# Kernel optimization log

Measured on AMD Instinct MI355X. Metric: run time of the kernel, lower is better.

The kernel has to match this reference:

```python
import jax, jax.numpy as jnp
import numpy as np

N_HEADS = 16
D_EMBED = 1024
D_HEAD = D_EMBED // N_HEADS
CAUSAL = False


def setup_inputs() -> dict:
    key = jax.random.key(0)
    k1, k2, k3, k4, k5 = jax.random.split(key, 5)
    B, S, D = 4, 2048, D_EMBED
    scale = 1.0 / np.sqrt(D)
    return {
        "x": jax.random.normal(k1, (B, S, D), dtype=jnp.float32),
        "w_in": jax.random.normal(k2, (D, 3 * D), dtype=jnp.float32) * scale,
        "b_in": jax.random.normal(k3, (3 * D,), dtype=jnp.float32) * 0.02,
        "w_out": jax.random.normal(k4, (D, D), dtype=jnp.float32) * scale,
        "b_out": jax.random.normal(k5, (D,), dtype=jnp.float32) * 0.02,
    }


def reference(x, w_in, b_in, w_out, b_out):
    B, S, D = x.shape
    qkv = jnp.einsum("bsd,de->bse", x, w_in) + b_in  # [B,S,3D]
    q, k, v = jnp.split(qkv, 3, axis=-1)
    # split heads -> [B,H,S,Dh]
    def sh(t):
        return t.reshape(B, S, N_HEADS, D_HEAD).transpose(0, 2, 1, 3)
    q, k, v = sh(q), sh(k), sh(v)
    weight = jnp.einsum("bhsd,bhtd->bhst", q, k)  # [B,H,S,S]
    if CAUSAL:
        mask = jnp.triu(jnp.ones((S, S), dtype=bool), k=1)
        weight = jnp.where(mask, -jnp.inf, weight)
    weight = weight / np.sqrt(D_HEAD)
    weight = jax.nn.softmax(weight, axis=-1)
    out = jnp.einsum("bhst,bhtd->bhsd", weight, v)
    out = out.transpose(0, 2, 1, 3).reshape(B, S, D)
    return jnp.einsum("bsd,de->bse", out, w_out) + b_out
```

## Files before the change

kernel.cpp:

```cpp
#include <hip/hip_runtime.h>
#include <hip/hip_bf16.h>

typedef unsigned short u16;
typedef __attribute__((ext_vector_type(8))) short bf16x8;
typedef __attribute__((ext_vector_type(4))) float f32x4;

#define QSCALE 0.180336880f

#define DEV static __device__ __forceinline__

DEV u16 f2bf(float f) {
  union { float f; unsigned u; } v; v.f = f;
  unsigned r = v.u + 0x7fffu + ((v.u >> 16) & 1u);
  return (u16)(r >> 16);
}

DEV unsigned pk2(float a, float b) {
  union { __hip_bfloat162 h; unsigned u; } c;
  c.h = __float22bfloat162_rn(make_float2(a, b));
  return c.u;
}

DEV void gll16(void* lds, const void* g) {
  __builtin_amdgcn_global_load_lds(
      (const __attribute__((address_space(1))) unsigned int*)g,
      (__attribute__((address_space(3))) unsigned int*)lds, 16, 0, 0);
}

DEV bf16x8 lds_swz_read(const u16* tile, int row, int colbyte) {
  const char* p = (const char*)tile + row * 128 + (colbyte ^ ((row & 7) << 4));
  return *(const bf16x8*)p;
}

DEV void stage_swz(u16* lds_tile, const u16* gbase, int gstride, int wave, int lane) {
#pragma unroll
  for (int j = 0; j < 2; ++j) {
    const int chunk = wave * 2 + j;
    const int a = chunk * 1024 + lane * 16;
    const int r = a >> 7;
    const int cb = (a & 127) ^ ((r & 7) << 4);
    gll16(lds_tile + chunk * 512, &gbase[(size_t)r * gstride + (cb >> 1)]);
  }
}

__global__ __launch_bounds__(256) void cvt_f32_to_bf16(const float* __restrict__ in,
                                                       u16* __restrict__ out, int n4) {
  int i = blockIdx.x * blockDim.x + threadIdx.x;
  int stride = gridDim.x * blockDim.x;
  for (; i < n4; i += stride) {
    float4 f = ((const float4*)in)[i];
    ushort4 u;
    u.x = f2bf(f.x); u.y = f2bf(f.y); u.z = f2bf(f.z); u.w = f2bf(f.w);
    ((ushort4*)out)[i] = u;
  }
}

__global__ __launch_bounds__(256) void transpose_cvt(const float* __restrict__ W,
                                                     u16* __restrict__ Wt,
                                                     int K, int N, int sn, float sval) {
  __shared__ u16 t[64][65];
  const int k0 = blockIdx.x * 64, n0 = blockIdx.y * 64;
  const int tid = threadIdx.x;
  const int rr = tid >> 4;
  const int cc = (tid & 15) * 4;
  const float scl = (n0 < sn) ? sval : 1.0f;
#pragma unroll
  for (int i = 0; i < 4; ++i) {
    const int row = rr * 4 + i;
    float4 f = *(const float4*)&W[(size_t)(k0 + row) * N + n0 + cc];
    t[row][cc + 0] = f2bf(f.x * scl);
    t[row][cc + 1] = f2bf(f.y * scl);
    t[row][cc + 2] = f2bf(f.z * scl);
    t[row][cc + 3] = f2bf(f.w * scl);
  }
  __syncthreads();
#pragma unroll
  for (int i = 0; i < 4; ++i) {
    const int n = rr * 4 + i;
    ushort4 u;
    u.x = t[cc + 0][n]; u.y = t[cc + 1][n]; u.z = t[cc + 2][n]; u.w = t[cc + 3][n];
    *(ushort4*)&Wt[(size_t)(n0 + n) * K + k0 + cc] = u;
  }
}

__global__ __launch_bounds__(256) void transpose_v(const u16* __restrict__ qkv,
                                                   u16* __restrict__ vT) {
  __shared__ u16 t[64][72];
  const int bh = blockIdx.y;
  const int b = bh >> 4, h = bh & 15;
  const int t0 = blockIdx.x * 64;
  const int tid = threadIdx.x;
  const int row = tid >> 2;
  const int cg = (tid & 3) * 16;
  const size_t src = (size_t)b * 2048 * 3072 + (size_t)(t0 + row) * 3072 + 2048 + h * 64 + cg;
  bf16x8 v0 = *(const bf16x8*)&qkv[src];
  bf16x8 v1 = *(const bf16x8*)&qkv[src + 8];
#pragma unroll
  for (int i = 0; i < 8; ++i) { t[row][cg + i] = (u16)v0[i]; t[row][cg + 8 + i] = (u16)v1[i]; }
  __syncthreads();
  const int d = tid >> 2;
  const int tg = (tid & 3) * 16;
  bf16x8 o0, o1;
#pragma unroll
  for (int i = 0; i < 8; ++i) { o0[i] = (short)t[tg + i][d]; o1[i] = (short)t[tg + 8 + i][d]; }
  u16* dst = &vT[((size_t)bh * 64 + d) * 2048 + t0 + tg];
  *(bf16x8*)dst = o0;
  *(bf16x8*)(dst + 8) = o1;
}

template<bool OUT_BF16>
__global__ __launch_bounds__(256) void gemm_bf16(const u16* __restrict__ A,
                                                 const u16* __restrict__ Bt,
                                                 const float* __restrict__ bias,
                                                 void* __restrict__ Cout,
                                                 int M, int N, int K, int qn) {
  __shared__ __align__(16) u16 As[128][64];
  __shared__ __align__(16) u16 Bs[128][64];
  const int tid = threadIdx.x;
  const int wave = tid >> 6, lane = tid & 63;
  const int g = lane >> 4, lr = lane & 15;
  const int bm = blockIdx.x * 128, bn = blockIdx.y * 128;
  const int wm = (wave >> 1) * 64, wn = (wave & 1) * 64;
  f32x4 acc[4][4] = {};
  for (int kt = 0; kt < K; kt += 64) {
    __syncthreads();
#pragma unroll
    for (int j = 0; j < 4; ++j) {
      int chunk = wave * 4 + j;
      int e = chunk * 512 + lane * 8;
      int r = e >> 6, c = e & 63;
      gll16((u16*)As + chunk * 512, &A[(size_t)(bm + r) * K + kt + c]);
      gll16((u16*)Bs + chunk * 512, &Bt[(size_t)(bn + r) * K + kt + c]);
    }
    __syncthreads();
#pragma unroll
    for (int kk = 0; kk < 64; kk += 32) {
      bf16x8 af[4], bfr[4];
#pragma unroll
      for (int m = 0; m < 4; ++m)
        af[m] = *(const bf16x8*)&As[wm + m * 16 + lr][kk + g * 8];
#pragma unroll
      for (int n = 0; n < 4; ++n)
        bfr[n] = *(const bf16x8*)&Bs[wn + n * 16 + lr][kk + g * 8];
#pragma unroll
      for (int m = 0; m < 4; ++m)
#pragma unroll
        for (int n = 0; n < 4; ++n)
          acc[m][n] = __builtin_amdgcn_mfma_f32_16x16x32_bf16(af[m], bfr[n], acc[m][n], 0, 0, 0);
    }
  }
#pragma unroll
  for (int m = 0; m < 4; ++m) {
#pragma unroll
    for (int n = 0; n < 4; ++n) {
      const int col = bn + wn + n * 16 + lr;
      float bv = bias ? bias[col] : 0.f;
      if (col < qn) bv *= QSCALE;
#pragma unroll
      for (int r = 0; r < 4; ++r) {
        const int row = bm + wm + m * 16 + g * 4 + r;
        float v = acc[m][n][r] + bv;
        if (OUT_BF16) ((u16*)Cout)[(size_t)row * N + col] = f2bf(v);
        else          ((float*)Cout)[(size_t)row * N + col] = v;
      }
    }
  }
}

__global__ __launch_bounds__(256) void attn_kernel(const u16* __restrict__ qkv,
                                                   const u16* __restrict__ vT,
                                                   u16* __restrict__ out) {
  __shared__ __align__(16) u16 Ks[2][4096];
  __shared__ __align__(16) u16 Vs[2][4096];
  __shared__ __align__(16) u16 Ps[4][1024];
  const int tid = threadIdx.x;
  const int wave = tid >> 6, lane = tid & 63;
  const int g = lane >> 4, lr = lane & 15;
  const int bh = blockIdx.y;
  const int b = bh >> 4, h = bh & 15;
  const int q0 = blockIdx.x * 64;
  const size_t base = (size_t)b * 2048 * 3072;
  const u16* kg = qkv + base + 1024 + h * 64;
  const u16* vg = vT + (size_t)bh * 64 * 2048;

  const int qrow = q0 + wave * 16 + lr;
  bf16x8 qf[2];
#pragma unroll
  for (int kk = 0; kk < 2; ++kk)
    qf[kk] = *(const bf16x8*)&qkv[base + (size_t)qrow * 3072 + h * 64 + kk * 32 + g * 8];

  f32x4 o[4] = {};
  float m = -1e30f, lsum = 0.f;

  stage_swz(Ks[0], kg, 3072, wave, lane);
  stage_swz(Vs[0], vg, 2048, wave, lane);
  __syncthreads();
  int cur = 0;
  char* const pwrow = (char*)Ps[wave] + lr * 128;
  const int psw = (lr & 7) << 4;
  for (int it = 0; it < 32; ++it) {
    if (it < 31) {
      stage_swz(Ks[cur ^ 1], kg + (size_t)(it + 1) * 64 * 3072, 3072, wave, lane);
      stage_swz(Vs[cur ^ 1], vg + (it + 1) * 64, 2048, wave, lane);
    }
    f32x4 s[4] = {};
#pragma unroll
    for (int kk = 0; kk < 2; ++kk)
#pragma unroll
      for (int n = 0; n < 4; ++n) {
        bf16x8 kf = lds_swz_read(Ks[cur], n * 16 + lr, kk * 64 + g * 16);
        s[n] = __builtin_amdgcn_mfma_f32_16x16x32_bf16(kf, qf[kk], s[n], 0, 0, 0);
      }
    f32x4 t01, t23;
#pragma unroll
    for (int i = 0; i < 4; ++i) {
      t01[i] = fmaxf(s[0][i], s[1][i]);
      t23[i] = fmaxf(s[2][i], s[3][i]);
    }
    f32x4 t = { fmaxf(t01[0], t23[0]), fmaxf(t01[1], t23[1]),
                fmaxf(t01[2], t23[2]), fmaxf(t01[3], t23[3]) };
    float pmax = fmaxf(fmaxf(t[0], t[1]), fmaxf(t[2], t[3]));
    if (!__all(pmax <= m + 8.f)) {
      float pm = fmaxf(pmax, __shfl_xor(pmax, 16));
      pm = fmaxf(pm, __shfl_xor(pm, 32));
      float mnew = fmaxf(m, pm);
      float sc = __builtin_amdgcn_exp2f(m - mnew);
      float sc0 = __shfl(sc, g * 4 + 0);
      float sc1 = __shfl(sc, g * 4 + 1);
      float sc2 = __shfl(sc, g * 4 + 2);
      float sc3 = __shfl(sc, g * 4 + 3);
#pragma unroll
      for (int nd = 0; nd < 4; ++nd) {
        o[nd][0] *= sc0; o[nd][1] *= sc1; o[nd][2] *= sc2; o[nd][3] *= sc3;
      }
      lsum *= sc;
      m = mnew;
    }
    float su = 0.f;
#pragma unroll
    for (int n = 0; n < 4; ++n) {
      float p0 = __builtin_amdgcn_exp2f(s[n][0] - m);
      float p1 = __builtin_amdgcn_exp2f(s[n][1] - m);
      float p2 = __builtin_amdgcn_exp2f(s[n][2] - m);
      float p3 = __builtin_amdgcn_exp2f(s[n][3] - m);
      uint2 w;
      w.x = pk2(p0, p1);
      w.y = pk2(p2, p3);
      *(uint2*)(pwrow + ((n * 32 + g * 8) ^ psw)) = w;
      su += (p0 + p1) + (p2 + p3);
    }
    lsum += su;
#pragma unroll
    for (int kk = 0; kk < 2; ++kk) {
      bf16x8 pf = lds_swz_read(Ps[wave], lr, kk * 64 + g * 16);
#pragma unroll
      for (int nd = 0; nd < 4; ++nd) {
        bf16x8 vf = lds_swz_read(Vs[cur], nd * 16 + lr, kk * 64 + g * 16);
        o[nd] = __builtin_amdgcn_mfma_f32_16x16x32_bf16(pf, vf, o[nd], 0, 0, 0);
      }
    }
    __syncthreads();
    cur ^= 1;
  }
  float lf = lsum + __shfl_xor(lsum, 16);
  lf += __shfl_xor(lf, 32);
  float l0 = __shfl(lf, g * 4 + 0);
  float l1 = __shfl(lf, g * 4 + 1);
  float l2 = __shfl(lf, g * 4 + 2);
  float l3 = __shfl(lf, g * 4 + 3);
  const size_t orow0 = (size_t)b * 2048 + q0 + wave * 16;
#pragma unroll
  for (int nd = 0; nd < 4; ++nd) {
    const int dcol = h * 64 + nd * 16 + lr;
    out[(orow0 + g * 4 + 0) * 1024 + dcol] = f2bf(o[nd][0] / l0);
    out[(orow0 + g * 4 + 1) * 1024 + dcol] = f2bf(o[nd][1] / l1);
    out[(orow0 + g * 4 + 2) * 1024 + dcol] = f2bf(o[nd][2] / l2);
    out[(orow0 + g * 4 + 3) * 1024 + dcol] = f2bf(o[nd][3] / l3);
  }
}

extern "C" void kernel_launch(void* const* d_in, const int* in_sizes, int n_in,
                              void* d_out, int out_size, void* d_ws, size_t ws_size,
                              hipStream_t stream) {
  (void)in_sizes; (void)n_in; (void)out_size; (void)ws_size;
  const float* x     = (const float*)d_in[0];
  const float* w_in  = (const float*)d_in[1];
  const float* b_in  = (const float*)d_in[2];
  const float* w_out = (const float*)d_in[3];
  const float* b_out = (const float*)d_in[4];
  float* out = (float*)d_out;

  char* ws = (char*)d_ws;
  u16* Xbf   = (u16*)ws; ws += (size_t)8192 * 1024 * 2;
  u16* WinT  = (u16*)ws; ws += (size_t)3072 * 1024 * 2;
  u16* WoutT = (u16*)ws; ws += (size_t)1024 * 1024 * 2;
  u16* qkv   = (u16*)ws; ws += (size_t)8192 * 3072 * 2;
  u16* attno = (u16*)ws; ws += (size_t)8192 * 1024 * 2;
  u16* vT    = Xbf;

  cvt_f32_to_bf16<<<2048, 256, 0, stream>>>(x, Xbf, 8192 * 1024 / 4);
  transpose_cvt<<<dim3(16, 48), 256, 0, stream>>>(w_in, WinT, 1024, 3072, 1024, QSCALE);
  transpose_cvt<<<dim3(16, 16), 256, 0, stream>>>(w_out, WoutT, 1024, 1024, 0, 1.0f);
  gemm_bf16<true ><<<dim3(64, 24), 256, 0, stream>>>(Xbf,   WinT,  b_in,  qkv, 8192, 3072, 1024, 1024);
  transpose_v<<<dim3(32, 64), 256, 0, stream>>>(qkv, vT);
  attn_kernel<<<dim3(32, 64), 256, 0, stream>>>(qkv, vT, attno);
  gemm_bf16<false><<<dim3(64, 8),  256, 0, stream>>>(attno, WoutT, b_out, out, 8192, 1024, 1024, 0);
}
```

Baseline: 265.0 us.

## Fuse V transpose into QKV GEMM epilogue and unroll attention loop by two

```diff
diff --git a/kernel.cpp b/kernel.cpp
--- a/kernel.cpp
+++ b/kernel.cpp
@@ -25,22 +25,6 @@
   __builtin_amdgcn_global_load_lds(
       (const __attribute__((address_space(1))) unsigned int*)g,
       (__attribute__((address_space(3))) unsigned int*)lds, 16, 0, 0);
-}
-
-DEV bf16x8 lds_swz_read(const u16* tile, int row, int colbyte) {
-  const char* p = (const char*)tile + row * 128 + (colbyte ^ ((row & 7) << 4));
-  return *(const bf16x8*)p;
-}
-
-DEV void stage_swz(u16* lds_tile, const u16* gbase, int gstride, int wave, int lane) {
-#pragma unroll
-  for (int j = 0; j < 2; ++j) {
-    const int chunk = wave * 2 + j;
-    const int a = chunk * 1024 + lane * 16;
-    const int r = a >> 7;
-    const int cb = (a & 127) ^ ((r & 7) << 4);
-    gll16(lds_tile + chunk * 512, &gbase[(size_t)r * gstride + (cb >> 1)]);
-  }
 }
 
 __global__ __launch_bounds__(256) void cvt_f32_to_bf16(const float* __restrict__ in,
@@ -113,7 +97,8 @@
                                                  const u16* __restrict__ Bt,
                                                  const float* __restrict__ bias,
                                                  void* __restrict__ Cout,
-                                                 int M, int N, int K, int qn) {
+                                                 int M, int N, int K, int qn,
+                                                 u16* __restrict__ vTout, int vn0) {
   __shared__ __align__(16) u16 As[128][64];
   __shared__ __align__(16) u16 Bs[128][64];
   const int tid = threadIdx.x;
@@ -156,16 +141,96 @@
       const int col = bn + wn + n * 16 + lr;
       float bv = bias ? bias[col] : 0.f;
       if (col < qn) bv *= QSCALE;
-#pragma unroll
-      for (int r = 0; r < 4; ++r) {
-        const int row = bm + wm + m * 16 + g * 4 + r;
-        float v = acc[m][n][r] + bv;
-        if (OUT_BF16) ((u16*)Cout)[(size_t)row * N + col] = f2bf(v);
-        else          ((float*)Cout)[(size_t)row * N + col] = v;
+      if (vTout != nullptr && col >= vn0) {
+        const int hc = col - vn0;
+#pragma unroll
+        for (int r = 0; r < 4; ++r) {
+          const int row = bm + wm + m * 16 + g * 4 + r;
+          const size_t idx = (((size_t)(row >> 11) * 16 + (hc >> 6)) * 64 + (hc & 63)) * 2048
+                             + (row & 2047);
+          vTout[idx] = f2bf(acc[m][n][r] + bv);
+        }
+      } else {
+#pragma unroll
+        for (int r = 0; r < 4; ++r) {
+          const int row = bm + wm + m * 16 + g * 4 + r;
+          float v = acc[m][n][r] + bv;
+          if (OUT_BF16) ((u16*)Cout)[(size_t)row * N + col] = f2bf(v);
+          else          ((float*)Cout)[(size_t)row * N + col] = v;
+        }
       }
     }
   }
 }
+
+
+#define ATTN_BODY(BUF, PRE)                                                     \
+  {                                                                             \
+    if (PRE) {                                                                  \
+      gll16((u16*)Ks[(BUF) ^ 1] + c0 * 512, gk0); gk0 += 64 * 3072;             \
+      gll16((u16*)Ks[(BUF) ^ 1] + c1 * 512, gk1); gk1 += 64 * 3072;             \
+      gll16((u16*)Vs[(BUF) ^ 1] + c0 * 512, gv0); gv0 += 64;                    \
+      gll16((u16*)Vs[(BUF) ^ 1] + c1 * 512, gv1); gv1 += 64;                    \
+    }                                                                           \
+    const char* kb = (const char*)Ks[(BUF)];                                    \
+    const char* vb = (const char*)Vs[(BUF)];                                    \
+    f32x4 s[4] = {};                                                            \
+    _Pragma("unroll")                                                           \
+    for (int kk = 0; kk < 2; ++kk)                                              \
+      _Pragma("unroll")                                                         \
+      for (int n = 0; n < 4; ++n) {                                             \
+        bf16x8 kf = *(const bf16x8*)(kb + off[kk][n]);                          \
+        s[n] = __builtin_amdgcn_mfma_f32_16x16x32_bf16(kf, qf[kk], s[n], 0, 0, 0); \
+      }                                                                         \
+    f32x4 t01, t23;                                                             \
+    _Pragma("unroll")                                                           \
+    for (int i = 0; i < 4; ++i) {                                               \
+      t01[i] = fmaxf(s[0][i], s[1][i]);                                         \
+      t23[i] = fmaxf(s[2][i], s[3][i]);                                         \
+    }                                                                           \
+    float pmax = fmaxf(fmaxf(fmaxf(t01[0], t23[0]), fmaxf(t01[1], t23[1])),     \
+                       fmaxf(fmaxf(t01[2], t23[2]), fmaxf(t01[3], t23[3])));    \
+    if (!__all(pmax <= m + 8.f)) {                                              \
+      float pm = fmaxf(pmax, __shfl_xor(pmax, 16));                             \
+      pm = fmaxf(pm, __shfl_xor(pm, 32));                                       \
+      float mnew = fmaxf(m, pm);                                                \
+      float sc = __builtin_amdgcn_exp2f(m - mnew);                              \
+      float sc0 = __shfl(sc, g * 4 + 0);                                        \
+      float sc1 = __shfl(sc, g * 4 + 1);                                        \
+      float sc2 = __shfl(sc, g * 4 + 2);                                        \
+      float sc3 = __shfl(sc, g * 4 + 3);                                        \
+      _Pragma("unroll")                                                         \
+      for (int nd = 0; nd < 4; ++nd) {                                          \
+        o[nd][0] *= sc0; o[nd][1] *= sc1; o[nd][2] *= sc2; o[nd][3] *= sc3;     \
+      }                                                                         \
+      lsum *= sc;                                                               \
+      m = mnew;                                                                 \
+    }                                                                           \
+    float su = 0.f;                                                             \
+    _Pragma("unroll")                                                           \
+    for (int n = 0; n < 4; ++n) {                                               \
+      float p0 = __builtin_amdgcn_exp2f(s[n][0] - m);                           \
+      float p1 = __builtin_amdgcn_exp2f(s[n][1] - m);                           \
+      float p2 = __builtin_amdgcn_exp2f(s[n][2] - m);                           \
+      float p3 = __builtin_amdgcn_exp2f(s[n][3] - m);                           \
+      uint2 w;                                                                  \
+      w.x = pk2(p0, p1);                                                        \
+      w.y = pk2(p2, p3);                                                        \
+      *(uint2*)(pb + pwo[n]) = w;                                               \
+      su += (p0 + p1) + (p2 + p3);                                              \
+    }                                                                           \
+    lsum += su;                                                                 \
+    _Pragma("unroll")                                                           \
+    for (int kk = 0; kk < 2; ++kk) {                                            \
+      bf16x8 pf = *(const bf16x8*)(pb + off[kk][0]);                            \
+      _Pragma("unroll")                                                         \
+      for (int nd = 0; nd < 4; ++nd) {                                          \
+        bf16x8 vf = *(const bf16x8*)(vb + off[kk][nd]);                         \
+        o[nd] = __builtin_amdgcn_mfma_f32_16x16x32_bf16(pf, vf, o[nd], 0, 0, 0); \
+      }                                                                         \
+    }                                                                           \
+    __syncthreads();                                                            \
+  }
 
 __global__ __launch_bounds__(256) void attn_kernel(const u16* __restrict__ qkv,
                                                    const u16* __restrict__ vT,
@@ -189,79 +254,42 @@
   for (int kk = 0; kk < 2; ++kk)
     qf[kk] = *(const bf16x8*)&qkv[base + (size_t)qrow * 3072 + h * 64 + kk * 32 + g * 8];
 
+  const int sw = (lr & 7) << 4;
+  int off[2][4];
+#pragma unroll
+  for (int kk = 0; kk < 2; ++kk)
+#pragma unroll
+    for (int n = 0; n < 4; ++n)
+      off[kk][n] = (n * 16 + lr) * 128 + ((kk * 64 + g * 16) ^ sw);
+  int pwo[4];
+#pragma unroll
+  for (int n = 0; n < 4; ++n)
+    pwo[n] = lr * 128 + ((n * 32 + g * 8) ^ sw);
+  char* const pb = (char*)Ps[wave];
+
+  const int c0 = wave * 2, c1 = c0 + 1;
+  const int a0 = c0 * 1024 + lane * 16, a1 = c1 * 1024 + lane * 16;
+  const int r0 = a0 >> 7, r1 = a1 >> 7;
+  const int cb0 = (a0 & 127) ^ ((r0 & 7) << 4), cb1 = (a1 & 127) ^ ((r1 & 7) << 4);
+  const u16* gk0 = kg + (size_t)r0 * 3072 + (cb0 >> 1);
+  const u16* gk1 = kg + (size_t)r1 * 3072 + (cb1 >> 1);
+  const u16* gv0 = vg + (size_t)r0 * 2048 + (cb0 >> 1);
+  const u16* gv1 = vg + (size_t)r1 * 2048 + (cb1 >> 1);
+
   f32x4 o[4] = {};
   float m = -1e30f, lsum = 0.f;
 
-  stage_swz(Ks[0], kg, 3072, wave, lane);
-  stage_swz(Vs[0], vg, 2048, wave, lane);
+  gll16((u16*)Ks[0] + c0 * 512, gk0); gk0 += 64 * 3072;
+  gll16((u16*)Ks[0] + c1 * 512, gk1); gk1 += 64 * 3072;
+  gll16((u16*)Vs[0] + c0 * 512, gv0); gv0 += 64;
+  gll16((u16*)Vs[0] + c1 * 512, gv1); gv1 += 64;
   __syncthreads();
-  int cur = 0;
-  char* const pwrow = (char*)Ps[wave] + lr * 128;
-  const int psw = (lr & 7) << 4;
-  for (int it = 0; it < 32; ++it) {
-    if (it < 31) {
-      stage_swz(Ks[cur ^ 1], kg + (size_t)(it + 1) * 64 * 3072, 3072, wave, lane);
-      stage_swz(Vs[cur ^ 1], vg + (it + 1) * 64, 2048, wave, lane);
-    }
-    f32x4 s[4] = {};
-#pragma unroll
-    for (int kk = 0; kk < 2; ++kk)
-#pragma unroll
-      for (int n = 0; n < 4; ++n) {
-        bf16x8 kf = lds_swz_read(Ks[cur], n * 16 + lr, kk * 64 + g * 16);
-        s[n] = __builtin_amdgcn_mfma_f32_16x16x32_bf16(kf, qf[kk], s[n], 0, 0, 0);
-      }
-    f32x4 t01, t23;
-#pragma unroll
-    for (int i = 0; i < 4; ++i) {
-      t01[i] = fmaxf(s[0][i], s[1][i]);
-      t23[i] = fmaxf(s[2][i], s[3][i]);
-    }
-    f32x4 t = { fmaxf(t01[0], t23[0]), fmaxf(t01[1], t23[1]),
-                fmaxf(t01[2], t23[2]), fmaxf(t01[3], t23[3]) };
-    float pmax = fmaxf(fmaxf(t[0], t[1]), fmaxf(t[2], t[3]));
-    if (!__all(pmax <= m + 8.f)) {
-      float pm = fmaxf(pmax, __shfl_xor(pmax, 16));
-      pm = fmaxf(pm, __shfl_xor(pm, 32));
-      float mnew = fmaxf(m, pm);
-      float sc = __builtin_amdgcn_exp2f(m - mnew);
-      float sc0 = __shfl(sc, g * 4 + 0);
-      float sc1 = __shfl(sc, g * 4 + 1);
-      float sc2 = __shfl(sc, g * 4 + 2);
-      float sc3 = __shfl(sc, g * 4 + 3);
-#pragma unroll
-      for (int nd = 0; nd < 4; ++nd) {
-        o[nd][0] *= sc0; o[nd][1] *= sc1; o[nd][2] *= sc2; o[nd][3] *= sc3;
-      }
-      lsum *= sc;
-      m = mnew;
-    }
-    float su = 0.f;
-#pragma unroll
-    for (int n = 0; n < 4; ++n) {
-      float p0 = __builtin_amdgcn_exp2f(s[n][0] - m);
-      float p1 = __builtin_amdgcn_exp2f(s[n][1] - m);
-      float p2 = __builtin_amdgcn_exp2f(s[n][2] - m);
-      float p3 = __builtin_amdgcn_exp2f(s[n][3] - m);
-      uint2 w;
-      w.x = pk2(p0, p1);
-      w.y = pk2(p2, p3);
-      *(uint2*)(pwrow + ((n * 32 + g * 8) ^ psw)) = w;
-      su += (p0 + p1) + (p2 + p3);
-    }
-    lsum += su;
-#pragma unroll
-    for (int kk = 0; kk < 2; ++kk) {
-      bf16x8 pf = lds_swz_read(Ps[wave], lr, kk * 64 + g * 16);
-#pragma unroll
-      for (int nd = 0; nd < 4; ++nd) {
-        bf16x8 vf = lds_swz_read(Vs[cur], nd * 16 + lr, kk * 64 + g * 16);
-        o[nd] = __builtin_amdgcn_mfma_f32_16x16x32_bf16(pf, vf, o[nd], 0, 0, 0);
-      }
-    }
-    __syncthreads();
-    cur ^= 1;
-  }
+
+  for (int it2 = 0; it2 < 16; ++it2) {
+    ATTN_BODY(0, 1)
+    ATTN_BODY(1, it2 < 15)
+  }
+
   float lf = lsum + __shfl_xor(lsum, 16);
   lf += __shfl_xor(lf, 32);
   float l0 = __shfl(lf, g * 4 + 0);
@@ -282,7 +310,7 @@
 extern "C" void kernel_launch(void* const* d_in, const int* in_sizes, int n_in,
                               void* d_out, int out_size, void* d_ws, size_t ws_size,
                               hipStream_t stream) {
-  (void)in_sizes; (void)n_in; (void)out_size; (void)ws_size;
+  (void)in_sizes; (void)n_in; (void)out_size;
   const float* x     = (const float*)d_in[0];
   const float* w_in  = (const float*)d_in[1];
   const float* b_in  = (const float*)d_in[2];
@@ -296,13 +324,24 @@
   u16* WoutT = (u16*)ws; ws += (size_t)1024 * 1024 * 2;
   u16* qkv   = (u16*)ws; ws += (size_t)8192 * 3072 * 2;
   u16* attno = (u16*)ws; ws += (size_t)8192 * 1024 * 2;
-  u16* vT    = Xbf;
+  u16* vTsep = (u16*)ws;
+
+  const size_t fused_need = 92274688ull + 16777216ull;
+  const bool fused = (ws_size >= fused_need);
+  u16* vT = fused ? vTsep : Xbf;
 
   cvt_f32_to_bf16<<<2048, 256, 0, stream>>>(x, Xbf, 8192 * 1024 / 4);
   transpose_cvt<<<dim3(16, 48), 256, 0, stream>>>(w_in, WinT, 1024, 3072, 1024, QSCALE);
   transpose_cvt<<<dim3(16, 16), 256, 0, stream>>>(w_out, WoutT, 1024, 1024, 0, 1.0f);
-  gemm_bf16<true ><<<dim3(64, 24), 256, 0, stream>>>(Xbf,   WinT,  b_in,  qkv, 8192, 3072, 1024, 1024);
-  transpose_v<<<dim3(32, 64), 256, 0, stream>>>(qkv, vT);
+  if (fused) {
+    gemm_bf16<true ><<<dim3(64, 24), 256, 0, stream>>>(Xbf, WinT, b_in, qkv,
+                                                       8192, 3072, 1024, 1024, vT, 2048);
+  } else {
+    gemm_bf16<true ><<<dim3(64, 24), 256, 0, stream>>>(Xbf, WinT, b_in, qkv,
+                                                       8192, 3072, 1024, 1024, nullptr, 1 << 30);
+    transpose_v<<<dim3(32, 64), 256, 0, stream>>>(qkv, vT);
+  }
   attn_kernel<<<dim3(32, 64), 256, 0, stream>>>(qkv, vT, attno);
-  gemm_bf16<false><<<dim3(64, 8),  256, 0, stream>>>(attno, WoutT, b_out, out, 8192, 1024, 1024, 0);
-}
+  gemm_bf16<false><<<dim3(64, 8), 256, 0, stream>>>(attno, WoutT, b_out, out,
+                                                    8192, 1024, 1024, 0, nullptr, 1 << 30);
+}
```

Result: faster. 253.2 us (-4.4%).
